# Kernel optimization log

Measured on AMD Instinct MI355X. Metric: run time of the kernel, lower is better.

The kernel has to match this reference:

```python
import jax, jax.numpy as jnp
import numpy as np

N, C_IN, H, W = 256, 256, 28, 28
D = 64        # prototype channel dim (prototype_shape[1])
P = 200       # num prototypes
NCLS = 10


def setup_inputs() -> dict:
    key = jax.random.key(0)
    ks = jax.random.split(key, 6)
    x = jax.random.normal(ks[0], (N, C_IN, H, W), dtype=jnp.float32)
    W1 = jax.random.normal(ks[1], (D, C_IN), dtype=jnp.float32) * 0.05
    b1 = jnp.zeros((D,), dtype=jnp.float32)
    W2 = jax.random.normal(ks[2], (D, D), dtype=jnp.float32) * 0.05
    b2 = jnp.zeros((D,), dtype=jnp.float32)
    prototypes = jax.random.uniform(ks[3], (P, D), dtype=jnp.float32)
    last_W = jax.random.normal(ks[4], (NCLS, P), dtype=jnp.float32) * 0.05
    last_b = jnp.zeros((NCLS,), dtype=jnp.float32)
    return {"x": x, "W1": W1, "b1": b1, "W2": W2, "b2": b2,
            "prototypes": prototypes, "last_W": last_W, "last_b": last_b}


def reference(x, W1, b1, W2, b2, prototypes, last_W, last_b):
    # add_on_layers: 1x1 conv -> relu -> 1x1 conv -> sigmoid (pointwise GEMMs)
    h = jax.nn.relu(jnp.einsum('nchw,oc->nohw', x, W1) + b1[None, :, None, None])
    f = jax.nn.sigmoid(jnp.einsum('nchw,oc->nohw', h, W2) + b2[None, :, None, None])
    # L2 convolution with 1x1 prototypes:
    # conv(x^2, ones) == channel sum of f^2, broadcast over P prototypes
    x2_patch_sum = jnp.sum(f * f, axis=1, keepdims=True)          # (N,1,H,W)
    xp = jnp.einsum('nchw,pc->nphw', f, prototypes)               # (N,P,H,W)
    p2 = jnp.sum(prototypes * prototypes, axis=1)[None, :, None, None]  # (1,P,1,1)
    distances = jax.nn.relu(x2_patch_sum - 2.0 * xp + p2)         # (N,P,H,W)
    # global min-pool over spatial dims (== -maxpool(-d) with full kernel)
    min_distances = jnp.min(distances, axis=(2, 3))               # (N,P)
    # paf == 'linear': similarity = -distance
    prototype_activations = -min_distances
    logits = prototype_activations @ last_W.T + last_b            # (N,NCLS)
    return (logits, min_distances)
```

## Files before the change

kernel.cpp:

```cpp
#include <hip/hip_runtime.h>
#include <hip/hip_bf16.h>

#define NIMG 256
#define CIN  256
#define PIX  784
#define DD   64
#define NP   200
#define NCLS 10

#define XS 264
#define HS 72

typedef __attribute__((ext_vector_type(8))) short bf16x8;
typedef __attribute__((ext_vector_type(4))) float f32x4;
typedef __attribute__((ext_vector_type(2))) unsigned int u32x2;

__device__ __forceinline__ unsigned short f2bf(float f) {
    union { float f; unsigned int u; } v; v.f = f;
    unsigned int r = v.u + 0x7fffu + ((v.u >> 16) & 1u);
    return (unsigned short)(r >> 16);
}
__device__ __forceinline__ unsigned int pk2(float a, float b) {
    __hip_bfloat162 p = __float22bfloat162_rn(make_float2(a, b));
    return *(unsigned int*)&p;
}

#define MFMA(a, b, c) __builtin_amdgcn_mfma_f32_16x16x32_bf16((a), (b), (c), 0, 0, 0)

__global__ __launch_bounds__(1024, 4)
void proto_fused_kernel(const float* __restrict__ x,
                        const float* __restrict__ W1, const float* __restrict__ b1,
                        const float* __restrict__ W2, const float* __restrict__ b2,
                        const float* __restrict__ proto,
                        const float* __restrict__ lastW, const float* __restrict__ lastb,
                        float* __restrict__ out)
{
    __shared__ __align__(16) unsigned short xlds[2][64 * XS];
    __shared__ __align__(16) unsigned short w1lds[64 * XS];
    __shared__ __align__(16) unsigned short htile[64 * HS];
    __shared__ __align__(16) unsigned short ftile[64 * HS];
    __shared__ float p2lds[208];
    __shared__ float b1lds[DD], b2lds[DD];
    __shared__ unsigned int bmin[208];

    const int n    = blockIdx.x;
    const int t    = threadIdx.x;
    const int lane = t & 63;
    const int wave = t >> 6;
    const int q    = lane >> 4;
    const int l15  = lane & 15;
    const int s    = wave & 3;
    const int dq   = wave >> 2;

    #pragma unroll
    for (int i = 0; i < 16; ++i) {
        int idx = t + i * 1024;
        w1lds[(idx >> 8) * XS + (idx & 255)] = f2bf(W1[idx]);
    }
    if (t < DD) { b1lds[t] = b1[t]; b2lds[t] = b2[t]; }
    if (t < 208) {
        float acc = 0.f;
        if (t < NP) {
            const float4* pp = (const float4*)(proto + t * DD);
            #pragma unroll
            for (int i = 0; i < 16; ++i) {
                float4 v = pp[i];
                acc += v.x * v.x + v.y * v.y + v.z * v.z + v.w * v.w;
            }
        }
        p2lds[t] = acc;
        bmin[t] = 0x7f800000u;
    }

    bf16x8 w2f[2];
    #pragma unroll
    for (int kk = 0; kk < 2; ++kk) {
        const float4* src = (const float4*)(W2 + (size_t)(dq * 16 + l15) * DD + kk * 32 + q * 8);
        float4 a = src[0], b = src[1];
        union { unsigned int u[4]; bf16x8 h; } cv;
        cv.u[0] = pk2(a.x, a.y); cv.u[1] = pk2(a.z, a.w);
        cv.u[2] = pk2(b.x, b.y); cv.u[3] = pk2(b.z, b.w);
        w2f[kk] = cv.h;
    }

    bf16x8 pb0[4], pb1[4];
    #pragma unroll
    for (int it = 0; it < 4; ++it) {
        int pt = dq + 4 * it;
        int p  = pt * 16 + l15;
        int pr = (pt < 13 && p < NP) ? p : (NP - 1);
        const float4* src = (const float4*)(proto + (size_t)pr * DD + q * 8);
        float4 a = src[0], b = src[1];
        float4 c = src[8], d = src[9];
        union { unsigned int u[4]; bf16x8 h; } c0, c1;
        c0.u[0] = pk2(a.x, a.y); c0.u[1] = pk2(a.z, a.w);
        c0.u[2] = pk2(b.x, b.y); c0.u[3] = pk2(b.z, b.w);
        c1.u[0] = pk2(c.x, c.y); c1.u[1] = pk2(c.z, c.w);
        c1.u[2] = pk2(d.x, d.y); c1.u[3] = pk2(d.z, d.w);
        pb0[it] = c0.h; pb1[it] = c1.h;
    }

    const int px4 = ((t >> 2) & 15) * 4;
    const int cgi = (t & 3) | ((t >> 6) << 2);
    const int c4  = cgi * 4;
    const int key = (px4 >> 2) & 3;
    const int choff = ((((cgi >> 1) ^ key) << 3) | ((cgi & 1) << 2));
    const float* xn = x + (size_t)n * CIN * PIX;

    float4 pf[4];
    auto load_tile = [&](int px0) {
        #pragma unroll
        for (int j = 0; j < 4; ++j) {
            const float* src = xn + (size_t)(c4 + j) * PIX + px0 + px4;
            float4 v;
            if (px0 + px4 + 3 < PIX) {
                v = *(const float4*)src;
            } else {
                v.x = (px0 + px4 + 0 < PIX) ? src[0] : 0.f;
                v.y = (px0 + px4 + 1 < PIX) ? src[1] : 0.f;
                v.z = (px0 + px4 + 2 < PIX) ? src[2] : 0.f;
                v.w = (px0 + px4 + 3 < PIX) ? src[3] : 0.f;
            }
            pf[j] = v;
        }
    };
    auto store_tile = [&](int buf) {
        #pragma unroll
        for (int r = 0; r < 4; ++r) {
            u32x2 uv;
            uv.x = pk2(((const float*)&pf[0])[r], ((const float*)&pf[1])[r]);
            uv.y = pk2(((const float*)&pf[2])[r], ((const float*)&pf[3])[r]);
            *(u32x2*)&xlds[buf][(px4 + r) * XS + choff] = uv;
        }
    };

    __syncthreads();

    bf16x8 w1f[8];
    #pragma unroll
    for (int kk = 0; kk < 8; ++kk)
        w1f[kk] = *(const bf16x8*)&w1lds[(dq * 16 + l15) * XS + kk * 32 + q * 8];
    const float b1r = b1lds[dq * 16 + l15];
    const float b2r = b2lds[dq * 16 + l15];
    float p2r[4];
    #pragma unroll
    for (int it = 0; it < 4; ++it) {
        int pt = dq + 4 * it;
        p2r[it] = p2lds[(pt < 13) ? (pt * 16 + l15) : 0];
    }
    float rmin[4];
    #pragma unroll
    for (int it = 0; it < 4; ++it) rmin[it] = 1e30f;

    const int rkey = l15 >> 2;

    load_tile(0);
    store_tile(0);
    load_tile(64);
    __syncthreads();

    for (int tl = 0; tl < 13; ++tl) {
        const int cur = tl & 1, nxt = cur ^ 1;

        if (tl < 12) store_tile(nxt);

        {
            f32x4 acc = {0.f, 0.f, 0.f, 0.f};
            const int arow = (s * 16 + l15) * XS;
            #pragma unroll
            for (int kk = 0; kk < 8; ++kk) {
                bf16x8 a = *(const bf16x8*)&xlds[cur][arow + (((kk * 4 + q) ^ rkey) << 3)];
                acc = MFMA(a, w1f[kk], acc);
            }
            #pragma unroll
            for (int r = 0; r < 4; ++r)
                htile[(s * 16 + q * 4 + r) * HS + dq * 16 + l15] =
                    f2bf(fmaxf(acc[r] + b1r, 0.f));
        }
        __syncthreads();

        {
            bf16x8 ha0 = *(const bf16x8*)&htile[(s * 16 + l15) * HS + q * 8];
            bf16x8 ha1 = *(const bf16x8*)&htile[(s * 16 + l15) * HS + 32 + q * 8];
            f32x4 acc2 = {0.f, 0.f, 0.f, 0.f};
            acc2 = MFMA(ha0, w2f[0], acc2);
            acc2 = MFMA(ha1, w2f[1], acc2);
            #pragma unroll
            for (int r = 0; r < 4; ++r) {
                float z = acc2[r] + b2r;
                float fvr = __builtin_amdgcn_rcpf(1.0f + __builtin_amdgcn_exp2f(z * -1.44269504f));
                ftile[(s * 16 + q * 4 + r) * HS + dq * 16 + l15] = f2bf(fvr);
            }
        }
        __syncthreads();

        if (tl < 11) load_tile((tl + 2) * 64);

        {
            bf16x8 fa0 = *(const bf16x8*)&ftile[(s * 16 + l15) * HS + q * 8];
            bf16x8 fa1 = *(const bf16x8*)&ftile[(s * 16 + l15) * HS + 32 + q * 8];

            f32x4 g = {0.f, 0.f, 0.f, 0.f};
            g = MFMA(fa0, fa0, g);
            g = MFMA(fa1, fa1, g);
            float s2v[4];
            #pragma unroll
            for (int r = 0; r < 4; ++r)
                s2v[r] = __shfl(g[r], 20 * q + r, 64);

            if (tl * 64 + s * 16 < PIX) {
                #pragma unroll
                for (int it = 0; it < 4; ++it) {
                    int pt = dq + 4 * it;
                    if (pt < 13) {
                        f32x4 a3 = {0.f, 0.f, 0.f, 0.f};
                        a3 = MFMA(fa0, pb0[it], a3);
                        a3 = MFMA(fa1, pb1[it], a3);
                        float m = 1e30f;
                        #pragma unroll
                        for (int r = 0; r < 4; ++r)
                            m = fminf(m, fmaxf(s2v[r] - 2.f * a3[r] + p2r[it], 0.f));
                        rmin[it] = fminf(rmin[it], m);
                    }
                }
            }
        }
    }

    #pragma unroll
    for (int it = 0; it < 4; ++it) {
        int pt = dq + 4 * it;
        if (pt < 13) {
            float m = rmin[it];
            m = fminf(m, __shfl_xor(m, 16, 64));
            m = fminf(m, __shfl_xor(m, 32, 64));
            if (lane < 16) atomicMin(&bmin[pt * 16 + l15], __float_as_uint(m));
        }
    }
    __syncthreads();

    if (t < NP) {
        out[NIMG * NCLS + (size_t)n * NP + t] = __uint_as_float(bmin[t]);
    }
    if (t < 320) {
        int c = t >> 5, j = t & 31;
        float acc = 0.f;
        for (int p = j; p < NP; p += 32)
            acc += __uint_as_float(bmin[p]) * lastW[c * NP + p];
        acc += __shfl_xor(acc, 1, 32);
        acc += __shfl_xor(acc, 2, 32);
        acc += __shfl_xor(acc, 4, 32);
        acc += __shfl_xor(acc, 8, 32);
        acc += __shfl_xor(acc, 16, 32);
        if (j == 0) out[(size_t)n * NCLS + c] = -acc + lastb[c];
    }
}

extern "C" void kernel_launch(void* const* d_in, const int* in_sizes, int n_in,
                              void* d_out, int out_size, void* d_ws, size_t ws_size,
                              hipStream_t stream) {
    const float* x     = (const float*)d_in[0];
    const float* W1    = (const float*)d_in[1];
    const float* b1    = (const float*)d_in[2];
    const float* W2    = (const float*)d_in[3];
    const float* b2    = (const float*)d_in[4];
    const float* proto = (const float*)d_in[5];
    const float* lastW = (const float*)d_in[6];
    const float* lastb = (const float*)d_in[7];
    float* out = (float*)d_out;

    proto_fused_kernel<<<dim3(NIMG), dim3(1024), 0, stream>>>(
        x, W1, b1, W2, b2, proto, lastW, lastb, out);
}
```

Baseline: 322.9 us.

## Load W1 fragments directly from global and deepen x prefetch to two tiles

Drops the W1 staging through LDS (and the b1/b2 LDS copies), so each wave reads its W1 MFMA fragments straight from global memory and converts them in registers. This removes about 33 KB of LDS and a round-trip through it. The x-tile prefetch now uses two register buffers, so loads run two tiles ahead and the first global loads are issued before the weight setup. The deeper prefetch raises register pressure and could lower occupancy or cause spills under the 1024-thread launch bound.

```diff
diff --git a/kernel.cpp b/kernel.cpp
--- a/kernel.cpp
+++ b/kernel.cpp
@@ -36,42 +36,66 @@
                         float* __restrict__ out)
 {
     __shared__ __align__(16) unsigned short xlds[2][64 * XS];
-    __shared__ __align__(16) unsigned short w1lds[64 * XS];
     __shared__ __align__(16) unsigned short htile[64 * HS];
     __shared__ __align__(16) unsigned short ftile[64 * HS];
     __shared__ float p2lds[208];
-    __shared__ float b1lds[DD], b2lds[DD];
     __shared__ unsigned int bmin[208];
 
     const int n    = blockIdx.x;
     const int t    = threadIdx.x;
     const int lane = t & 63;
-    const int wave = t >> 6;
     const int q    = lane >> 4;
     const int l15  = lane & 15;
-    const int s    = wave & 3;
-    const int dq   = wave >> 2;
-
-    #pragma unroll
-    for (int i = 0; i < 16; ++i) {
-        int idx = t + i * 1024;
-        w1lds[(idx >> 8) * XS + (idx & 255)] = f2bf(W1[idx]);
-    }
-    if (t < DD) { b1lds[t] = b1[t]; b2lds[t] = b2[t]; }
-    if (t < 208) {
-        float acc = 0.f;
-        if (t < NP) {
-            const float4* pp = (const float4*)(proto + t * DD);
-            #pragma unroll
-            for (int i = 0; i < 16; ++i) {
-                float4 v = pp[i];
-                acc += v.x * v.x + v.y * v.y + v.z * v.z + v.w * v.w;
-            }
-        }
-        p2lds[t] = acc;
-        bmin[t] = 0x7f800000u;
-    }
-
+    const int s    = (t >> 6) & 3;
+    const int dq   = t >> 8;
+
+    const int px4 = ((t >> 2) & 15) * 4;
+    const int cgi = (t & 3) | ((t >> 6) << 2);
+    const int c4  = cgi * 4;
+    const int key = (px4 >> 2) & 3;
+    const int choff = ((((cgi >> 1) ^ key) << 3) | ((cgi & 1) << 2));
+    const float* xn = x + (size_t)n * CIN * PIX;
+
+    float4 pf[2][4];
+    auto load_tile = [&](int buf, int px0) {
+        #pragma unroll
+        for (int j = 0; j < 4; ++j) {
+            const float* src = xn + (size_t)(c4 + j) * PIX + px0 + px4;
+            float4 v;
+            if (px0 + px4 + 3 < PIX) {
+                v = *(const float4*)src;
+            } else {
+                v.x = (px0 + px4 + 0 < PIX) ? src[0] : 0.f;
+                v.y = (px0 + px4 + 1 < PIX) ? src[1] : 0.f;
+                v.z = (px0 + px4 + 2 < PIX) ? src[2] : 0.f;
+                v.w = (px0 + px4 + 3 < PIX) ? src[3] : 0.f;
+            }
+            pf[buf][j] = v;
+        }
+    };
+    auto store_tile = [&](int buf, int dst) {
+        #pragma unroll
+        for (int r = 0; r < 4; ++r) {
+            u32x2 uv;
+            uv.x = pk2(((const float*)&pf[buf][0])[r], ((const float*)&pf[buf][1])[r]);
+            uv.y = pk2(((const float*)&pf[buf][2])[r], ((const float*)&pf[buf][3])[r]);
+            *(u32x2*)&xlds[dst][(px4 + r) * XS + choff] = uv;
+        }
+    };
+
+    load_tile(0, 0);
+    load_tile(1, 64);
+
+    bf16x8 w1f[8];
+    #pragma unroll
+    for (int kk = 0; kk < 8; ++kk) {
+        const float4* src = (const float4*)(W1 + (size_t)(dq * 16 + l15) * CIN + kk * 32 + q * 8);
+        float4 a = src[0], b = src[1];
+        union { unsigned int u[4]; bf16x8 h; } cv;
+        cv.u[0] = pk2(a.x, a.y); cv.u[1] = pk2(a.z, a.w);
+        cv.u[2] = pk2(b.x, b.y); cv.u[3] = pk2(b.z, b.w);
+        w1f[kk] = cv.h;
+    }
     bf16x8 w2f[2];
     #pragma unroll
     for (int kk = 0; kk < 2; ++kk) {
@@ -82,7 +106,6 @@
         cv.u[2] = pk2(b.x, b.y); cv.u[3] = pk2(b.z, b.w);
         w2f[kk] = cv.h;
     }
-
     bf16x8 pb0[4], pb1[4];
     #pragma unroll
     for (int it = 0; it < 4; ++it) {
@@ -99,49 +122,24 @@
         c1.u[2] = pk2(d.x, d.y); c1.u[3] = pk2(d.z, d.w);
         pb0[it] = c0.h; pb1[it] = c1.h;
     }
-
-    const int px4 = ((t >> 2) & 15) * 4;
-    const int cgi = (t & 3) | ((t >> 6) << 2);
-    const int c4  = cgi * 4;
-    const int key = (px4 >> 2) & 3;
-    const int choff = ((((cgi >> 1) ^ key) << 3) | ((cgi & 1) << 2));
-    const float* xn = x + (size_t)n * CIN * PIX;
-
-    float4 pf[4];
-    auto load_tile = [&](int px0) {
-        #pragma unroll
-        for (int j = 0; j < 4; ++j) {
-            const float* src = xn + (size_t)(c4 + j) * PIX + px0 + px4;
-            float4 v;
-            if (px0 + px4 + 3 < PIX) {
-                v = *(const float4*)src;
-            } else {
-                v.x = (px0 + px4 + 0 < PIX) ? src[0] : 0.f;
-                v.y = (px0 + px4 + 1 < PIX) ? src[1] : 0.f;
-                v.z = (px0 + px4 + 2 < PIX) ? src[2] : 0.f;
-                v.w = (px0 + px4 + 3 < PIX) ? src[3] : 0.f;
-            }
-            pf[j] = v;
-        }
-    };
-    auto store_tile = [&](int buf) {
-        #pragma unroll
-        for (int r = 0; r < 4; ++r) {
-            u32x2 uv;
-            uv.x = pk2(((const float*)&pf[0])[r], ((const float*)&pf[1])[r]);
-            uv.y = pk2(((const float*)&pf[2])[r], ((const float*)&pf[3])[r]);
-            *(u32x2*)&xlds[buf][(px4 + r) * XS + choff] = uv;
-        }
-    };
-
+    const float b1r = b1[dq * 16 + l15];
+    const float b2r = b2[dq * 16 + l15];
+
+    if (t < 208) {
+        float acc = 0.f;
+        if (t < NP) {
+            const float4* pp = (const float4*)(proto + t * DD);
+            #pragma unroll
+            for (int i = 0; i < 16; ++i) {
+                float4 v = pp[i];
+                acc += v.x * v.x + v.y * v.y + v.z * v.z + v.w * v.w;
+            }
+        }
+        p2lds[t] = acc;
+        bmin[t] = 0x7f800000u;
+    }
     __syncthreads();
 
-    bf16x8 w1f[8];
-    #pragma unroll
-    for (int kk = 0; kk < 8; ++kk)
-        w1f[kk] = *(const bf16x8*)&w1lds[(dq * 16 + l15) * XS + kk * 32 + q * 8];
-    const float b1r = b1lds[dq * 16 + l15];
-    const float b2r = b2lds[dq * 16 + l15];
     float p2r[4];
     #pragma unroll
     for (int it = 0; it < 4; ++it) {
@@ -154,15 +152,17 @@
 
     const int rkey = l15 >> 2;
 
-    load_tile(0);
-    store_tile(0);
-    load_tile(64);
+    store_tile(0, 0);
+    load_tile(0, 128);
     __syncthreads();
 
     for (int tl = 0; tl < 13; ++tl) {
         const int cur = tl & 1, nxt = cur ^ 1;
 
-        if (tl < 12) store_tile(nxt);
+        if (tl < 12) {
+            store_tile(nxt, nxt);
+            if (tl < 10) load_tile(nxt, (tl + 3) * 64);
+        }
 
         {
             f32x4 acc = {0.f, 0.f, 0.f, 0.f};
@@ -193,8 +193,6 @@
             }
         }
         __syncthreads();
-
-        if (tl < 11) load_tile((tl + 2) * 64);
 
         {
             bf16x8 fa0 = *(const bf16x8*)&ftile[(s * 16 + l15) * HS + q * 8];
```

Measured after the change: 398.0 us. +23.2%, slower.
